# Kernel tuning notes

Measured on AMD Instinct MI355X. Metric: run time of the kernel, lower is better.

The kernel has to match this reference:

```python
import jax, jax.numpy as jnp
import numpy as np

SAMPLING_RATE = 0.5

def setup_inputs() -> dict:
    key = jax.random.key(0)
    k1, k2 = jax.random.split(key)
    token = jax.random.normal(k1, (8, 16, 4, 384), dtype=jnp.float32)
    feature = jax.random.normal(k2, (8, 16, 4, 196, 384), dtype=jnp.float32)
    return {"token": token, "feature": feature}

def reference(token, feature):
    b1, n1, kk1, c = token.shape
    b2, n2, kk2, hw, _ = feature.shape
    N = n1 * kk1  # == n2 * kk2
    tok = token.reshape(b1, N, 1, c)           # [b, N, 1, c]
    feat = feature.reshape(b2, N, hw, c)       # [b, N, hw, c]
    scale = c ** (-0.5)
    # attention scores: [b, N, 1, hw]
    attn = jnp.einsum('bnqc,bnhc->bnqh', tok, feat) * scale
    attn = jax.nn.softmax(attn, axis=-1)
    tk = int(hw * SAMPLING_RATE)
    sel_attn, sel_idx = jax.lax.top_k(attn, tk)          # [b, N, 1, tk]
    sel_attn = sel_attn / jnp.sum(sel_attn, axis=-1, keepdims=True)
    # gather selected features: idx [b, N, tk] -> feat rows [b, N, tk, c]
    idx = sel_idx[:, :, 0, :]                            # [b, N, tk]
    sel_feat = jnp.take_along_axis(feat, idx[..., None], axis=2)  # [b, N, tk, c]
    out = jnp.einsum('bnqt,bntc->bnqc', sel_attn, sel_feat)       # [b, N, 1, c]
    return out.reshape(b1, n1, kk1, c)
```

## Files before the change

### kernel.cpp

```cpp
#include <hip/hip_runtime.h>

#define HW 196
#define C  384
#define CF4 (C/4)
#define TK 98
#define NT 512
#define NWAVE (NT/64)

__global__ __launch_bounds__(NT, 4) void sampling_kernel(
    const float* __restrict__ token,
    const float* __restrict__ feature,
    float* __restrict__ out)
{
    __shared__ float tokLds[C];
    __shared__ float score[HW];
    __shared__ float selW[TK];
    __shared__ int   selIdx[TK];
    __shared__ float wsum[NWAVE];
    __shared__ float part[NWAVE][C];
    __shared__ float s_max, s_winv;

    const int tid  = threadIdx.x;
    const int wave = tid >> 6;
    const int lane = tid & 63;
    const int g    = lane >> 2;
    const int l    = lane & 3;
    const int pair = blockIdx.x;

    const float* tokp  = token   + (size_t)pair * C;
    const float* featp = feature + (size_t)pair * (HW * C);
    const float4* f4base = (const float4*)featp;
    const float4* t4     = (const float4*)tokLds;

    for (int i = tid; i < C; i += NT) tokLds[i] = tokp[i];
    __syncthreads();

    const float scale = 0.05103103630798288f;

    #pragma unroll
    for (int strip = 0; strip < 2; ++strip) {
        const int r = strip * 128 + wave * 16 + g;
        if (r < HW) {
            const float4* f4 = f4base + (size_t)r * CF4;
            float4 acc = make_float4(0.f, 0.f, 0.f, 0.f);
            #pragma unroll
            for (int k = 0; k < 24; ++k) {
                float4 a = f4[l + 4 * k];
                float4 t = t4[l + 4 * k];
                acc.x += a.x * t.x; acc.y += a.y * t.y;
                acc.z += a.z * t.z; acc.w += a.w * t.w;
            }
            float s = (acc.x + acc.y) + (acc.z + acc.w);
            s += __shfl_xor(s, 1, 64);
            s += __shfl_xor(s, 2, 64);
            if (l == 0) score[r] = s * scale;
        }
    }
    __syncthreads();

    if (wave == 0) {
        float m = -3.4e38f;
        for (int i = lane; i < HW; i += 64) m = fmaxf(m, score[i]);
        #pragma unroll
        for (int off = 32; off > 0; off >>= 1)
            m = fmaxf(m, __shfl_xor(m, off, 64));
        if (lane == 0) s_max = m;
    }
    __syncthreads();

    float w = 0.f;
    if (tid < HW) {
        const float si = score[tid];
        int rank = 0;
        for (int j = 0; j < HW; ++j) {
            const float sj = score[j];
            rank += (int)((sj > si) | ((sj == si) & (j < tid)));
        }
        if (rank < TK) {
            w = __expf(si - s_max);
            selIdx[rank] = tid;
            selW[rank]  = w;
        }
    }
    #pragma unroll
    for (int off = 32; off > 0; off >>= 1) w += __shfl_xor(w, off, 64);
    if (lane == 0) wsum[wave] = w;
    __syncthreads();
    if (tid == 0) {
        float s = 0.f;
        #pragma unroll
        for (int i = 0; i < NWAVE; ++i) s += wsum[i];
        s_winv = 1.f / s;
    }
    __syncthreads();

    float4 acc_a = make_float4(0.f, 0.f, 0.f, 0.f);
    float4 acc_b = make_float4(0.f, 0.f, 0.f, 0.f);
    for (int base = wave; base < TK; base += 4 * NWAVE) {
        #pragma unroll
        for (int j = 0; j < 4; ++j) {
            const int i = base + j * NWAVE;
            if (i < TK) {
                const int   r   = selIdx[i];
                const float wgt = selW[i];
                const float4* f4 = f4base + (size_t)r * CF4;
                float4 a = f4[lane];
                acc_a.x += wgt * a.x; acc_a.y += wgt * a.y;
                acc_a.z += wgt * a.z; acc_a.w += wgt * a.w;
                if (lane < 32) {
                    float4 b = f4[64 + lane];
                    acc_b.x += wgt * b.x; acc_b.y += wgt * b.y;
                    acc_b.z += wgt * b.z; acc_b.w += wgt * b.w;
                }
            }
        }
    }
    float4* pw = (float4*)&part[wave][0];
    pw[lane] = acc_a;
    if (lane < 32) pw[64 + lane] = acc_b;
    __syncthreads();

    if (tid < C) {
        float s = 0.f;
        #pragma unroll
        for (int wv = 0; wv < NWAVE; ++wv) s += part[wv][tid];
        out[(size_t)pair * C + tid] = s * s_winv;
    }
}

extern "C" void kernel_launch(void* const* d_in, const int* in_sizes, int n_in,
                              void* d_out, int out_size, void* d_ws, size_t ws_size,
                              hipStream_t stream) {
    const float* token   = (const float*)d_in[0];
    const float* feature = (const float*)d_in[1];
    float* out = (float*)d_out;
    const int pairs = in_sizes[0] / C;
    sampling_kernel<<<pairs, NT, 0, stream>>>(token, feature, out);
}
```

Baseline: 39.14 us.

## Batch feature loads in score pass, split rank counting, fully unroll gather

The score pass now issues all 24 float4 loads of a row into registers before any FMAs, with a sched_barrier in between, so more memory requests are in flight. The O(HW^2) rank computation is split across 392 threads, each counting half of the comparisons, and a spare wave computes the max concurrently. The weighted gather loop is fully unrolled to 12 iterations plus a tail so more loads can be overlapped. This raises register pressure, which may reduce occupancy under the launch bounds of 4.

```diff
diff --git a/kernel.cpp b/kernel.cpp
--- a/kernel.cpp
+++ b/kernel.cpp
@@ -17,6 +17,7 @@
     __shared__ float selW[TK];
     __shared__ int   selIdx[TK];
     __shared__ float wsum[NWAVE];
+    __shared__ int   rank2[2 * HW];
     __shared__ float part[NWAVE][C];
     __shared__ float s_max, s_winv;
 
@@ -37,28 +38,73 @@
 
     const float scale = 0.05103103630798288f;
 
-    #pragma unroll
-    for (int strip = 0; strip < 2; ++strip) {
-        const int r = strip * 128 + wave * 16 + g;
-        if (r < HW) {
-            const float4* f4 = f4base + (size_t)r * CF4;
-            float4 acc = make_float4(0.f, 0.f, 0.f, 0.f);
+    {
+        const int r0 = wave * 16 + g;
+        const float4* f0 = f4base + (size_t)r0 * CF4 + l;
+        float4 a[12], b[12];
+        #pragma unroll
+        for (int k = 0; k < 12; ++k) a[k] = f0[4 * k];
+        #pragma unroll
+        for (int k = 0; k < 12; ++k) b[k] = f0[4 * (k + 12)];
+        __builtin_amdgcn_sched_barrier(0);
+        float4 acc = make_float4(0.f, 0.f, 0.f, 0.f);
+        #pragma unroll
+        for (int k = 0; k < 12; ++k) {
+            float4 t = t4[l + 4 * k];
+            acc.x += a[k].x * t.x; acc.y += a[k].y * t.y;
+            acc.z += a[k].z * t.z; acc.w += a[k].w * t.w;
+        }
+        #pragma unroll
+        for (int k = 0; k < 12; ++k) {
+            float4 t = t4[l + 4 * (k + 12)];
+            acc.x += b[k].x * t.x; acc.y += b[k].y * t.y;
+            acc.z += b[k].z * t.z; acc.w += b[k].w * t.w;
+        }
+        float s = (acc.x + acc.y) + (acc.z + acc.w);
+        s += __shfl_xor(s, 1, 64);
+        s += __shfl_xor(s, 2, 64);
+        if (l == 0) score[r0] = s * scale;
+
+        if (r0 < HW - 128) {
+            const int r1 = 128 + r0;
+            const float4* f1 = f4base + (size_t)r1 * CF4 + l;
             #pragma unroll
-            for (int k = 0; k < 24; ++k) {
-                float4 a = f4[l + 4 * k];
+            for (int k = 0; k < 12; ++k) a[k] = f1[4 * k];
+            #pragma unroll
+            for (int k = 0; k < 12; ++k) b[k] = f1[4 * (k + 12)];
+            __builtin_amdgcn_sched_barrier(0);
+            float4 acc1 = make_float4(0.f, 0.f, 0.f, 0.f);
+            #pragma unroll
+            for (int k = 0; k < 12; ++k) {
                 float4 t = t4[l + 4 * k];
-                acc.x += a.x * t.x; acc.y += a.y * t.y;
-                acc.z += a.z * t.z; acc.w += a.w * t.w;
+                acc1.x += a[k].x * t.x; acc1.y += a[k].y * t.y;
+                acc1.z += a[k].z * t.z; acc1.w += a[k].w * t.w;
             }
-            float s = (acc.x + acc.y) + (acc.z + acc.w);
-            s += __shfl_xor(s, 1, 64);
-            s += __shfl_xor(s, 2, 64);
-            if (l == 0) score[r] = s * scale;
+            #pragma unroll
+            for (int k = 0; k < 12; ++k) {
+                float4 t = t4[l + 4 * (k + 12)];
+                acc1.x += b[k].x * t.x; acc1.y += b[k].y * t.y;
+                acc1.z += b[k].z * t.z; acc1.w += b[k].w * t.w;
+            }
+            float s1 = (acc1.x + acc1.y) + (acc1.z + acc1.w);
+            s1 += __shfl_xor(s1, 1, 64);
+            s1 += __shfl_xor(s1, 2, 64);
+            if (l == 0) score[r1] = s1 * scale;
         }
     }
     __syncthreads();
 
-    if (wave == 0) {
+    if (tid < 2 * HW) {
+        const int i = tid >> 1, h = tid & 1;
+        const float si = score[i];
+        int cnt = 0;
+        const int j0 = h * (HW / 2);
+        for (int j = j0; j < j0 + HW / 2; ++j) {
+            const float sj = score[j];
+            cnt += (int)((sj > si) | ((sj == si) & (j < i)));
+        }
+        rank2[tid] = cnt;
+    } else if (wave == NWAVE - 1) {
         float m = -3.4e38f;
         for (int i = lane; i < HW; i += 64) m = fmaxf(m, score[i]);
         #pragma unroll
@@ -70,14 +116,9 @@
 
     float w = 0.f;
     if (tid < HW) {
-        const float si = score[tid];
-        int rank = 0;
-        for (int j = 0; j < HW; ++j) {
-            const float sj = score[j];
-            rank += (int)((sj > si) | ((sj == si) & (j < tid)));
-        }
+        const int rank = rank2[2 * tid] + rank2[2 * tid + 1];
         if (rank < TK) {
-            w = __expf(si - s_max);
+            w = __expf(score[tid] - s_max);
             selIdx[rank] = tid;
             selW[rank]  = w;
         }
@@ -96,23 +137,33 @@
 
     float4 acc_a = make_float4(0.f, 0.f, 0.f, 0.f);
     float4 acc_b = make_float4(0.f, 0.f, 0.f, 0.f);
-    for (int base = wave; base < TK; base += 4 * NWAVE) {
-        #pragma unroll
-        for (int j = 0; j < 4; ++j) {
-            const int i = base + j * NWAVE;
-            if (i < TK) {
-                const int   r   = selIdx[i];
-                const float wgt = selW[i];
-                const float4* f4 = f4base + (size_t)r * CF4;
-                float4 a = f4[lane];
-                acc_a.x += wgt * a.x; acc_a.y += wgt * a.y;
-                acc_a.z += wgt * a.z; acc_a.w += wgt * a.w;
-                if (lane < 32) {
-                    float4 b = f4[64 + lane];
-                    acc_b.x += wgt * b.x; acc_b.y += wgt * b.y;
-                    acc_b.z += wgt * b.z; acc_b.w += wgt * b.w;
-                }
-            }
+    #pragma unroll
+    for (int j = 0; j < 12; ++j) {
+        const int i = wave + NWAVE * j;
+        const int   r   = selIdx[i];
+        const float wgt = selW[i];
+        const float4* f4 = f4base + (size_t)r * CF4;
+        float4 aa = f4[lane];
+        acc_a.x += wgt * aa.x; acc_a.y += wgt * aa.y;
+        acc_a.z += wgt * aa.z; acc_a.w += wgt * aa.w;
+        if (lane < 32) {
+            float4 bb = f4[64 + lane];
+            acc_b.x += wgt * bb.x; acc_b.y += wgt * bb.y;
+            acc_b.z += wgt * bb.z; acc_b.w += wgt * bb.w;
+        }
+    }
+    if (wave < TK - 96) {
+        const int i = 96 + wave;
+        const int   r   = selIdx[i];
+        const float wgt = selW[i];
+        const float4* f4 = f4base + (size_t)r * CF4;
+        float4 aa = f4[lane];
+        acc_a.x += wgt * aa.x; acc_a.y += wgt * aa.y;
+        acc_a.z += wgt * aa.z; acc_a.w += wgt * aa.w;
+        if (lane < 32) {
+            float4 bb = f4[64 + lane];
+            acc_b.x += wgt * bb.x; acc_b.y += wgt * bb.y;
+            acc_b.z += wgt * bb.z; acc_b.w += wgt * bb.w;
         }
     }
     float4* pw = (float4*)&part[wave][0];
```

After: 38.50 us. Within noise of the previous version (-1.7%).
